# Kernel tuning notes

Measured on AMD Instinct MI355X. Metric: run time of the kernel, lower is better.

Reference implementation:

```python
import jax, jax.numpy as jnp
import numpy as np
from jax import lax

# module constants (from init_kwargs)
IN_CH = 128
OUT_CH = 128
CTX = 128
KS = 3
STRIDE = 1
PAD = 1
GROUPS = 1
ATT_GROUPS = 1
K = 4
TEMP = 30.0  # T_max, used as the fixed temperature at init


def setup_inputs() -> dict:
    key = jax.random.key(0)
    k1, k2, k3, k4, k5 = jax.random.split(key, 5)
    b, f, t = 16, 64, 256
    x = jax.random.normal(k1, (b, IN_CH, f, t), dtype=jnp.float32)
    g = jax.random.normal(k2, (1, b, CTX), dtype=jnp.float32)
    # Dense(k*att_groups) params (kaiming-normal kernel, zero bias)
    fan_in = CTX
    dense_kernel = jax.random.normal(k3, (CTX, K * ATT_GROUPS), dtype=jnp.float32) * np.sqrt(2.0 / fan_in)
    dense_bias = jnp.zeros((K * ATT_GROUPS,), dtype=jnp.float32)
    # kernel bank: (k, out, in//groups, ks, ks) -> swapaxes(1,2) -> flatten to (1, att_groups, k, -1)
    flat = OUT_CH * (IN_CH // GROUPS) * KS * KS // ATT_GROUPS
    weight = jax.random.normal(k4, (1, ATT_GROUPS, K, flat), dtype=jnp.float32) * np.sqrt(2.0 / flat)
    return {"x": x, "g": g, "dense_kernel": dense_kernel, "dense_bias": dense_bias, "weight": weight}


def reference(x, g, dense_kernel, dense_bias, weight):
    b, c, f, t = x.shape
    g_c = g[0].reshape(b, -1)                                  # [b, ctx]
    residuals = (g_c @ dense_kernel + dense_bias).reshape(b, ATT_GROUPS, 1, -1)  # [b, ag, 1, k]
    attention = jax.nn.softmax(residuals / TEMP, axis=-1)      # [b, ag, 1, k]
    # per-sample kernel aggregation: [b, ag, 1, k] @ [1, ag, k, D] -> [b, ag, 1, D]
    agg = (attention @ weight).swapaxes(1, 2)                  # [b, 1, ag, D]
    agg = agg.reshape(b * OUT_CH, IN_CH // GROUPS, KS, KS)
    # batch-as-groups grouped conv
    out = lax.conv_general_dilated(
        x.reshape(1, b * c, f, t), agg,
        window_strides=(STRIDE, STRIDE),
        padding=[(PAD, PAD), (PAD, PAD)],
        dimension_numbers=("NCHW", "OIHW", "NCHW"),
        feature_group_count=b * GROUPS,
    )
    return out.reshape(b, OUT_CH, out.shape[-2], out.shape[-1])
```

## Files before the change

kernel.cpp:

```cpp
#include <hip/hip_runtime.h>
#include <stdint.h>

#define NB 16
#define NC 128
#define NOC 128
#define NF 64
#define NT 256
#define NCTX 128
#define NTAPS 9
#define NFLAT 147456
#define TEMPR 30.0f

#define SXCOLS 130
#define SXSTRIDE 131
#define SX_CH (12*SXSTRIDE)

typedef float f32x4 __attribute__((ext_vector_type(4)));
typedef __bf16 bf16x8 __attribute__((ext_vector_type(8)));

__global__ void attn_kernel(const float* __restrict__ g,
                            const float* __restrict__ dk,
                            const float* __restrict__ bias,
                            float* __restrict__ att) {
    int b = threadIdx.x;
    if (b >= NB) return;
    float r0 = bias[0], r1 = bias[1], r2 = bias[2], r3 = bias[3];
    const float* gb = g + b * NCTX;
    for (int c = 0; c < NCTX; ++c) {
        float gv = gb[c];
        r0 += gv * dk[c*4+0];
        r1 += gv * dk[c*4+1];
        r2 += gv * dk[c*4+2];
        r3 += gv * dk[c*4+3];
    }
    r0 *= (1.0f/TEMPR); r1 *= (1.0f/TEMPR); r2 *= (1.0f/TEMPR); r3 *= (1.0f/TEMPR);
    float mx = fmaxf(fmaxf(r0, r1), fmaxf(r2, r3));
    float e0 = expf(r0-mx), e1 = expf(r1-mx), e2 = expf(r2-mx), e3 = expf(r3-mx);
    float s = e0+e1+e2+e3;
    att[b*4+0] = e0/s; att[b*4+1] = e1/s; att[b*4+2] = e2/s; att[b*4+3] = e3/s;
}

__global__ void agg_kernel(const float* __restrict__ w,
                           const float* __restrict__ att,
                           unsigned short* __restrict__ wb) {
    int idx = blockIdx.x * 256 + threadIdx.x;
    int ic = idx & 127;
    int oc = (idx >> 7) & 127;
    int b  = idx >> 14;
    float a0 = att[b*4+0], a1 = att[b*4+1], a2 = att[b*4+2], a3 = att[b*4+3];
    int d0 = (oc*NC + ic) * NTAPS;
    int c4 = ic >> 5;
    int kq = (ic >> 3) & 3;
    int e  = ic & 7;
    #pragma unroll
    for (int tap = 0; tap < NTAPS; ++tap) {
        float s = a0 * w[0*NFLAT + d0 + tap]
                + a1 * w[1*NFLAT + d0 + tap]
                + a2 * w[2*NFLAT + d0 + tap]
                + a3 * w[3*NFLAT + d0 + tap];
        __bf16 h = (__bf16)s;
        unsigned short u = *(unsigned short*)&h;
        int chunk = (tap * 4 + kq) * 128 + oc;
        wb[(((b * 4 + c4) * (NTAPS*4*NOC)) + chunk) * 8 + e] = u;
    }
}

__global__ __launch_bounds__(256) void conv_kernel(
        const float* __restrict__ x,
        const unsigned short* __restrict__ wb,
        float* __restrict__ out) {
    __shared__ __align__(16) unsigned short sx[SX_CH * 8];

    const int p_  = blockIdx.x;
    const int lg  = (p_ & 7) * 256 + (p_ >> 3);
    const int b   = lg >> 7;
    const int y   = (lg >> 1) & 63;
    const int t0  = (lg & 1) * 128;

    const int tid  = threadIdx.x;
    const int lane = tid & 63;
    const int wid  = tid >> 6;
    const int wpix = wid & 1;
    const int woc  = wid >> 1;
    const int l15  = lane & 15;
    const int l4   = lane >> 4;

    f32x4 acc[4][4];
    #pragma unroll
    for (int m = 0; m < 4; ++m)
        #pragma unroll
        for (int n = 0; n < 4; ++n)
            acc[m][n] = (f32x4){0.f, 0.f, 0.f, 0.f};

    const float* xb = x + (b * NC) * (NF * NT);
    const unsigned short* const wbase =
        wb + b * (NTAPS * NOC * NC) + (l4 * 128 + woc * 64 + l15) * 8;
    const unsigned short* const sxp = sx + (l4 * SXSTRIDE + wpix * 64 + l15) * 8;

    const int se  = tid & 3;
    const int skq = (tid >> 2) & 3;

    f32x4 xv0[6], xv1[6];
    float bf0 = 0.f, bf1 = 0.f;
    bf16x8 A0[4], A1[4];

    auto issue_x = [&](int c4) {
        const int ic = c4 * 32 + skq * 8 + se * 2;
        #pragma unroll
        for (int j = 0; j < 6; ++j) {
            const int u = tid + j * 256;
            const int q = (u >> 4) & 31;
            const int r = u >> 9;
            const int iy = y - 1 + r;
            f32x4 v0 = (f32x4){0.f,0.f,0.f,0.f};
            f32x4 v1 = v0;
            if ((unsigned)iy < (unsigned)NF) {
                const float* src = xb + (ic * NF + iy) * NT + t0 + q * 4;
                v0 = *(const f32x4*)src;
                v1 = *(const f32x4*)(src + NF * NT);
            }
            xv0[j] = v0;
            xv1[j] = v1;
        }
        bf0 = 0.f; bf1 = 0.f;
        if (tid < 96) {
            const int side = (tid >> 4) & 1;
            const int r    = tid >> 5;
            const int t    = side ? (t0 + 128) : (t0 - 1);
            const int iy   = y - 1 + r;
            if ((unsigned)iy < (unsigned)NF && (unsigned)t < (unsigned)NT) {
                const float* src = xb + (ic * NF + iy) * NT + t;
                bf0 = src[0];
                bf1 = src[NF * NT];
            }
        }
    };

    auto write_x = [&]() {
        #pragma unroll
        for (int j = 0; j < 6; ++j) {
            const int u = tid + j * 256;
            const int q = (u >> 4) & 31;
            const int r = u >> 9;
            unsigned short* dst =
                sx + ((r * 4 + skq) * SXSTRIDE + q * 4 + 1) * 8 + se * 2;
            #pragma unroll
            for (int jj = 0; jj < 4; ++jj) {
                __bf16 h0 = (__bf16)xv0[j][jj];
                __bf16 h1 = (__bf16)xv1[j][jj];
                unsigned pk = (unsigned)*(unsigned short*)&h0
                            | ((unsigned)*(unsigned short*)&h1 << 16);
                *(unsigned*)(dst + jj * 8) = pk;
            }
        }
        if (tid < 96) {
            const int side = (tid >> 4) & 1;
            const int r    = tid >> 5;
            const int col  = side ? (SXCOLS - 1) : 0;
            __bf16 h0 = (__bf16)bf0;
            __bf16 h1 = (__bf16)bf1;
            unsigned pk = (unsigned)*(unsigned short*)&h0
                        | ((unsigned)*(unsigned short*)&h1 << 16);
            *(unsigned*)(sx + ((r * 4 + skq) * SXSTRIDE + col) * 8 + se * 2) = pk;
        }
    };

    auto loadA = [&](bf16x8* dst, int c4, int tap) {
        const unsigned short* wt = wbase + (c4 * NTAPS + tap) * 4096;
        dst[0] = *(const bf16x8*)(wt);
        dst[1] = *(const bf16x8*)(wt + 128);
        dst[2] = *(const bf16x8*)(wt + 256);
        dst[3] = *(const bf16x8*)(wt + 384);
    };

#define DO_TAP(KY, KX, A) do {                                                 \
        bf16x8 bfv[4];                                                         \
        _Pragma("unroll")                                                      \
        for (int n = 0; n < 4; ++n)                                            \
            bfv[n] = *(const bf16x8*)(sxp +                                    \
                        ((KY)*4*SXSTRIDE + (KX) + n*16) * 8);                  \
        _Pragma("unroll")                                                      \
        for (int m = 0; m < 4; ++m)                                            \
            _Pragma("unroll")                                                  \
            for (int n = 0; n < 4; ++n)                                        \
                acc[m][n] = __builtin_amdgcn_mfma_f32_16x16x32_bf16(           \
                    A[m], bfv[n], acc[m][n], 0, 0, 0);                         \
    } while (0)

    issue_x(0);
    loadA(A0, 0, 0);
    loadA(A1, 0, 1);
    write_x();
    __syncthreads();

    for (int c4 = 0; c4 < 4; ++c4) {
        if (c4 < 3) issue_x(c4 + 1);

        DO_TAP(0, 0, A0); loadA(A0, c4, 2);
        DO_TAP(0, 1, A1); loadA(A1, c4, 3);
        DO_TAP(0, 2, A0); loadA(A0, c4, 4);
        DO_TAP(1, 0, A1); loadA(A1, c4, 5);
        DO_TAP(1, 1, A0); loadA(A0, c4, 6);
        DO_TAP(1, 2, A1); loadA(A1, c4, 7);
        DO_TAP(2, 0, A0); loadA(A0, c4, 8);
        DO_TAP(2, 1, A1);
        DO_TAP(2, 2, A0);

        if (c4 < 3) {
            loadA(A0, c4 + 1, 0);
            loadA(A1, c4 + 1, 1);
            __syncthreads();
            write_x();
            __syncthreads();
        }
    }
#undef DO_TAP

    #pragma unroll
    for (int m = 0; m < 4; ++m) {
        int ocb = woc * 64 + m * 16 + l4 * 4;
        #pragma unroll
        for (int r = 0; r < 4; ++r) {
            float* orow = out + ((b * NOC + ocb + r) * NF + y) * NT + t0;
            #pragma unroll
            for (int n = 0; n < 4; ++n)
                orow[wpix * 64 + n * 16 + l15] = acc[m][n][r];
        }
    }
}

extern "C" void kernel_launch(void* const* d_in, const int* in_sizes, int n_in,
                              void* d_out, int out_size, void* d_ws, size_t ws_size,
                              hipStream_t stream) {
    const float* x    = (const float*)d_in[0];
    const float* g    = (const float*)d_in[1];
    const float* dk   = (const float*)d_in[2];
    const float* bias = (const float*)d_in[3];
    const float* w    = (const float*)d_in[4];
    float* out = (float*)d_out;

    float* att = (float*)d_ws;
    unsigned short* wb = (unsigned short*)((char*)d_ws + 256);

    attn_kernel<<<dim3(1), dim3(64), 0, stream>>>(g, dk, bias, att);
    agg_kernel<<<dim3(1024), dim3(256), 0, stream>>>(w, att, wb);
    conv_kernel<<<dim3(2048), dim3(256), 0, stream>>>(x, wb, out);
}
```

Measured before the change: 135.5 us.

## Drop x register prefetch and raise conv kernel occupancy to four blocks per CU

Removes the register-held software prefetch of the next input-channel chunk of x, which held 48 floats per thread. Each chunk is now loaded and written to shared memory directly between barriers. Launch bounds now request 4 blocks per CU, so more waves are resident to hide global-load latency in place of the explicit prefetch. The risk is exposed load latency on every chunk if the extra waves do not cover it.

After: 175.4 us. +29.5%, slower.

```diff
diff --git a/kernel.cpp b/kernel.cpp
--- a/kernel.cpp
+++ b/kernel.cpp
@@ -65,7 +65,7 @@
     }
 }
 
-__global__ __launch_bounds__(256) void conv_kernel(
+__global__ __launch_bounds__(256, 4) void conv_kernel(
         const float* __restrict__ x,
         const unsigned short* __restrict__ wb,
         float* __restrict__ out) {
@@ -100,11 +100,17 @@
     const int se  = tid & 3;
     const int skq = (tid >> 2) & 3;
 
-    f32x4 xv0[6], xv1[6];
-    float bf0 = 0.f, bf1 = 0.f;
     bf16x8 A0[4], A1[4];
 
-    auto issue_x = [&](int c4) {
+    auto loadA = [&](bf16x8* dst, int c4, int tap) {
+        const unsigned short* wt = wbase + (c4 * NTAPS + tap) * 4096;
+        dst[0] = *(const bf16x8*)(wt);
+        dst[1] = *(const bf16x8*)(wt + 128);
+        dst[2] = *(const bf16x8*)(wt + 256);
+        dst[3] = *(const bf16x8*)(wt + 384);
+    };
+
+    auto stage_x = [&](int c4) {
         const int ic = c4 * 32 + skq * 8 + se * 2;
         #pragma unroll
         for (int j = 0; j < 6; ++j) {
@@ -119,35 +125,12 @@
                 v0 = *(const f32x4*)src;
                 v1 = *(const f32x4*)(src + NF * NT);
             }
-            xv0[j] = v0;
-            xv1[j] = v1;
-        }
-        bf0 = 0.f; bf1 = 0.f;
-        if (tid < 96) {
-            const int side = (tid >> 4) & 1;
-            const int r    = tid >> 5;
-            const int t    = side ? (t0 + 128) : (t0 - 1);
-            const int iy   = y - 1 + r;
-            if ((unsigned)iy < (unsigned)NF && (unsigned)t < (unsigned)NT) {
-                const float* src = xb + (ic * NF + iy) * NT + t;
-                bf0 = src[0];
-                bf1 = src[NF * NT];
-            }
-        }
-    };
-
-    auto write_x = [&]() {
-        #pragma unroll
-        for (int j = 0; j < 6; ++j) {
-            const int u = tid + j * 256;
-            const int q = (u >> 4) & 31;
-            const int r = u >> 9;
             unsigned short* dst =
                 sx + ((r * 4 + skq) * SXSTRIDE + q * 4 + 1) * 8 + se * 2;
             #pragma unroll
             for (int jj = 0; jj < 4; ++jj) {
-                __bf16 h0 = (__bf16)xv0[j][jj];
-                __bf16 h1 = (__bf16)xv1[j][jj];
+                __bf16 h0 = (__bf16)v0[jj];
+                __bf16 h1 = (__bf16)v1[jj];
                 unsigned pk = (unsigned)*(unsigned short*)&h0
                             | ((unsigned)*(unsigned short*)&h1 << 16);
                 *(unsigned*)(dst + jj * 8) = pk;
@@ -156,21 +139,21 @@
         if (tid < 96) {
             const int side = (tid >> 4) & 1;
             const int r    = tid >> 5;
+            const int t    = side ? (t0 + 128) : (t0 - 1);
+            const int iy   = y - 1 + r;
             const int col  = side ? (SXCOLS - 1) : 0;
-            __bf16 h0 = (__bf16)bf0;
-            __bf16 h1 = (__bf16)bf1;
+            float f0 = 0.f, f1 = 0.f;
+            if ((unsigned)iy < (unsigned)NF && (unsigned)t < (unsigned)NT) {
+                const float* src = xb + (ic * NF + iy) * NT + t;
+                f0 = src[0];
+                f1 = src[NF * NT];
+            }
+            __bf16 h0 = (__bf16)f0;
+            __bf16 h1 = (__bf16)f1;
             unsigned pk = (unsigned)*(unsigned short*)&h0
                         | ((unsigned)*(unsigned short*)&h1 << 16);
             *(unsigned*)(sx + ((r * 4 + skq) * SXSTRIDE + col) * 8 + se * 2) = pk;
         }
-    };
-
-    auto loadA = [&](bf16x8* dst, int c4, int tap) {
-        const unsigned short* wt = wbase + (c4 * NTAPS + tap) * 4096;
-        dst[0] = *(const bf16x8*)(wt);
-        dst[1] = *(const bf16x8*)(wt + 128);
-        dst[2] = *(const bf16x8*)(wt + 256);
-        dst[3] = *(const bf16x8*)(wt + 384);
     };
 
 #define DO_TAP(KY, KX, A) do {                                                 \
@@ -187,14 +170,12 @@
                     A[m], bfv[n], acc[m][n], 0, 0, 0);                         \
     } while (0)
 
-    issue_x(0);
-    loadA(A0, 0, 0);
-    loadA(A1, 0, 1);
-    write_x();
-    __syncthreads();
-
     for (int c4 = 0; c4 < 4; ++c4) {
-        if (c4 < 3) issue_x(c4 + 1);
+        loadA(A0, c4, 0);
+        loadA(A1, c4, 1);
+        __syncthreads();
+        stage_x(c4);
+        __syncthreads();
 
         DO_TAP(0, 0, A0); loadA(A0, c4, 2);
         DO_TAP(0, 1, A1); loadA(A1, c4, 3);
@@ -205,14 +186,6 @@
         DO_TAP(2, 0, A0); loadA(A0, c4, 8);
         DO_TAP(2, 1, A1);
         DO_TAP(2, 2, A0);
-
-        if (c4 < 3) {
-            loadA(A0, c4 + 1, 0);
-            loadA(A1, c4 + 1, 1);
-            __syncthreads();
-            write_x();
-            __syncthreads();
-        }
     }
 #undef DO_TAP
 
```
